# Optimization experiments

Hardware: AMD Instinct MI355X
Metric: run time of the kernel (lower is better)

The kernel has to match this reference:

```python
import jax, jax.numpy as jnp
import numpy as np

D_MODEL = 1024
N_HEADS = 16
D_KEYS = 64
D_LLM = 4096
B, L, S = 8, 1024, 1000
HD = N_HEADS * D_KEYS  # 1024


def setup_inputs() -> dict:
    key = jax.random.key(0)
    ks = jax.random.split(key, 12)
    sd = lambda fan_in: 1.0 / np.sqrt(fan_in)
    return {
        "target_embedding": jax.random.normal(ks[0], (B, L, D_MODEL), jnp.float32),
        "source_embedding": jax.random.normal(ks[1], (S, D_LLM), jnp.float32),
        "value_embedding": jax.random.normal(ks[2], (S, D_LLM), jnp.float32),
        "Wq": jax.random.normal(ks[3], (D_MODEL, HD), jnp.float32) * sd(D_MODEL),
        "bq": jnp.zeros((HD,), jnp.float32),
        "Wk": jax.random.normal(ks[4], (D_LLM, HD), jnp.float32) * sd(D_LLM),
        "bk": jnp.zeros((HD,), jnp.float32),
        "Wv": jax.random.normal(ks[5], (D_LLM, HD), jnp.float32) * sd(D_LLM),
        "bv": jnp.zeros((HD,), jnp.float32),
        "Wo": jax.random.normal(ks[6], (HD, D_LLM), jnp.float32) * sd(HD),
        "bo": jnp.zeros((D_LLM,), jnp.float32),
        "alpha": jnp.asarray(1.0, jnp.float32),
        "beta": jnp.asarray(0.5, jnp.float32),
    }


def reference(target_embedding, source_embedding, value_embedding,
              Wq, bq, Wk, bk, Wv, bv, Wo, bo, alpha, beta):
    # Projections
    q = (target_embedding @ Wq + bq).reshape(B, L, N_HEADS, D_KEYS)   # blhe
    k = (source_embedding @ Wk + bk).reshape(S, N_HEADS, D_KEYS)      # she
    v = (value_embedding @ Wv + bv).reshape(S, N_HEADS, D_KEYS)       # she
    # Reprogramming attention with alpha/beta scaling
    scale = 1.0 / np.sqrt(D_KEYS)
    scores = jnp.einsum('blhe,she->bhls', alpha * q, beta * k)        # BxHxLxS
    A = jax.nn.softmax(scale * scores, axis=-1)  # dropout is identity in eval
    out = jnp.einsum('bhls,she->blhe', A, v)
    out = out.reshape(B, L, HD)
    return out @ Wo + bo                                              # B,L,d_llm
```

## Files before the change

### kernel.cpp

```cpp
#include <hip/hip_runtime.h>

typedef unsigned short u16;
typedef __attribute__((ext_vector_type(8))) short short8;
typedef __attribute__((ext_vector_type(4))) float floatx4;

#define LOG2E 1.4426950408889634f

__device__ __forceinline__ u16 f2bf(float f) {
    unsigned u = __builtin_bit_cast(unsigned, f);
    u += 0x7fffu + ((u >> 16) & 1u);
    return (u16)(u >> 16);
}

__device__ __forceinline__ void gl2lds16(const void* g, void* l) {
    __builtin_amdgcn_global_load_lds((const __attribute__((address_space(1))) void*)g,
                                     (__attribute__((address_space(3))) void*)l,
                                     16, 0, 0);
}

__global__ __launch_bounds__(256) void conv_all(const float* __restrict__ T, u16* __restrict__ Tb,
                                                const float* __restrict__ Se, u16* __restrict__ Seb,
                                                const float* __restrict__ Ve, u16* __restrict__ Veb) {
    int g = blockIdx.x * 256 + threadIdx.x;
    const float* s; u16* d; int i; int nsrc;
    if (g < 2097152)      { s = T;  d = Tb;  i = g * 4;               nsrc = 8388608; }
    else if (g < 3145728) { s = Se; d = Seb; i = (g - 2097152) * 4;   nsrc = 4096000; }
    else                  { s = Ve; d = Veb; i = (g - 3145728) * 4;   nsrc = 4096000; }
    ushort4 o;
    if (i < nsrc) {
        float4 v = *(const float4*)(s + i);
        o.x = f2bf(v.x); o.y = f2bf(v.y); o.z = f2bf(v.z); o.w = f2bf(v.w);
    } else {
        o = make_ushort4(0, 0, 0, 0);
    }
    *(ushort4*)(d + i) = o;
}

__device__ __forceinline__ void transpose_core(const float* __restrict__ W, u16* __restrict__ Wt,
                                               int Kd, int Nd, int kx, int ny) {
    __shared__ u16 t[64][65];
    const int tid = threadIdx.x;
    const int k0 = kx * 64, n0 = ny * 64;
#pragma unroll
    for (int i = 0; i < 16; i++) {
        int r = i * 4 + (tid >> 6), c = tid & 63;
        t[r][c] = f2bf(W[(size_t)(k0 + r) * Nd + n0 + c]);
    }
    __syncthreads();
#pragma unroll
    for (int i = 0; i < 16; i++) {
        int n = i * 4 + (tid >> 6), k = tid & 63;
        Wt[(size_t)(n0 + n) * Kd + k0 + k] = t[k][n];
    }
}

__global__ __launch_bounds__(256) void transpose3(const float* __restrict__ Wq, u16* __restrict__ WqT,
                                                  const float* __restrict__ Wk, u16* __restrict__ WkT,
                                                  const float* __restrict__ Wv, u16* __restrict__ WvT) {
    int id = blockIdx.x;
    if (id < 256)       transpose_core(Wq, WqT, 1024, 1024, id & 15, id >> 4);
    else if (id < 1280) { int t = id - 256;  transpose_core(Wk, WkT, 4096, 1024, t & 63, t >> 6); }
    else                { int t = id - 1280; transpose_core(Wv, WvT, 4096, 1024, t & 63, t >> 6); }
}

__device__ __forceinline__
void gemm_core(const u16* __restrict__ A, const u16* __restrict__ Bt,
               const float* __restrict__ bias, void* __restrict__ Cout,
               int M, int N, int Kstride, int Klen, int koff,
               int mode, float mult, int m0, int n0,
               u16* sA, u16* sB) {
    const int tid = threadIdx.x;
    const int wave = tid >> 6, lane = tid & 63;
    const int quad = lane >> 4, l16 = lane & 15;
    const int wm = (wave >> 1) * 64, wn = (wave & 1) * 64;

    floatx4 acc[4][4];
#pragma unroll
    for (int i = 0; i < 4; i++)
#pragma unroll
        for (int j = 0; j < 4; j++) acc[i][j] = (floatx4){0.f, 0.f, 0.f, 0.f};

    const u16* Ag = A + (size_t)m0 * Kstride + koff;
    const u16* Bg = Bt + (size_t)n0 * Kstride + koff;
    const int sr = tid >> 3, sc = (tid & 7) * 8;

    for (int k0 = 0; k0 < Klen; k0 += 64) {
#pragma unroll
        for (int i = 0; i < 4; i++) {
            int r = i * 32 + sr;
            gl2lds16(Ag + (size_t)r * Kstride + k0 + sc, sA + i * 2048 + wave * 512);
            gl2lds16(Bg + (size_t)r * Kstride + k0 + sc, sB + i * 2048 + wave * 512);
        }
        __syncthreads();
#pragma unroll
        for (int kk = 0; kk < 64; kk += 32) {
            short8 af[4], bf[4];
#pragma unroll
            for (int i = 0; i < 4; i++)
                af[i] = *(const short8*)&sA[(wm + i * 16 + l16) * 64 + kk + quad * 8];
#pragma unroll
            for (int j = 0; j < 4; j++)
                bf[j] = *(const short8*)&sB[(wn + j * 16 + l16) * 64 + kk + quad * 8];
#pragma unroll
            for (int i = 0; i < 4; i++)
#pragma unroll
                for (int j = 0; j < 4; j++)
                    acc[i][j] = __builtin_amdgcn_mfma_f32_16x16x32_bf16(af[i], bf[j], acc[i][j], 0, 0, 0);
        }
        __syncthreads();
    }

#pragma unroll
    for (int i = 0; i < 4; i++) {
#pragma unroll
        for (int j = 0; j < 4; j++) {
            int col = n0 + wn + j * 16 + l16;
            float bv = (mode >= 4) ? 0.0f : bias[col];
#pragma unroll
            for (int r = 0; r < 4; r++) {
                int row = m0 + wm + i * 16 + quad * 4 + r;
                float v = (acc[i][j][r] + bv) * mult;
                if (mode == 3 || mode == 4) {
                    ((float*)Cout)[(size_t)row * N + col] = v;
                } else if (mode == 5) {
                    ((float*)Cout)[(size_t)col * M + row] = v;
                } else if (mode == 2) {
                    ((u16*)Cout)[(size_t)col * M + row] = f2bf(v);
                } else {
                    ((u16*)Cout)[(size_t)row * N + col] = f2bf(v);
                }
            }
        }
    }
}

__global__ __launch_bounds__(256, 2)
void gemm_qkv(const u16* __restrict__ Tb, const u16* __restrict__ WqT, const float* __restrict__ bq,
              const u16* __restrict__ Seb, const u16* __restrict__ WkT,
              const u16* __restrict__ Veb, const u16* __restrict__ WvT,
              u16* __restrict__ Qb, float* __restrict__ KP, float* __restrict__ VPT,
              const float* __restrict__ alphaP, const float* __restrict__ betaP) {
    __shared__ u16 sA[128 * 64];
    __shared__ u16 sB[128 * 64];
    int b0 = blockIdx.x;
    int bid = (b0 & 7) * 128 + (b0 >> 3);
    if (bid < 512) {
        int m = bid >> 3, n = bid & 7;
        float mult = alphaP[0] * betaP[0] * 0.125f * LOG2E;
        gemm_core(Tb, WqT, bq, Qb, 8192, 1024, 1024, 1024, 0,
                  1, mult, m * 128, n * 128, sA, sB);
    } else if (bid < 768) {
        int t = bid - 512;
        int kc = t >> 6, m = (t >> 3) & 7, n = t & 7;
        gemm_core(Seb, WkT, nullptr, KP + (size_t)kc * 1048576, 1024, 1024, 4096, 1024, kc * 1024,
                  4, 1.0f, m * 128, n * 128, sA, sB);
    } else {
        int t = bid - 768;
        int kc = t >> 6, m = (t >> 3) & 7, n = t & 7;
        gemm_core(Veb, WvT, nullptr, VPT + (size_t)kc * 1048576, 1024, 1024, 4096, 1024, kc * 1024,
                  5, 1.0f, m * 128, n * 128, sA, sB);
    }
}

__global__ __launch_bounds__(256)
void reduce_wo(const float* __restrict__ KP, const float* __restrict__ bk, u16* __restrict__ Kb,
               const float* __restrict__ VPT, const float* __restrict__ bv, u16* __restrict__ VTb,
               const float* __restrict__ Wo, u16* __restrict__ WoT) {
    int id = blockIdx.x;
    if (id >= 2048) {
        int t = id - 2048;
        transpose_core(Wo, WoT, 1024, 4096, t & 15, t >> 4);
        return;
    }
    const int tid = threadIdx.x;
    if (id < 1024) {
        int r = id, c = tid * 4;
        size_t base = (size_t)r * 1024 + c;
        float4 a0 = *(const float4*)(KP + base);
        float4 a1 = *(const float4*)(KP + 1048576 + base);
        float4 a2 = *(const float4*)(KP + 2097152 + base);
        float4 a3 = *(const float4*)(KP + 3145728 + base);
        float4 bb = *(const float4*)(bk + c);
        ushort4 o;
        o.x = f2bf(a0.x + a1.x + a2.x + a3.x + bb.x);
        o.y = f2bf(a0.y + a1.y + a2.y + a3.y + bb.y);
        o.z = f2bf(a0.z + a1.z + a2.z + a3.z + bb.z);
        o.w = f2bf(a0.w + a1.w + a2.w + a3.w + bb.w);
        *(ushort4*)(Kb + base) = o;
    } else {
        int d = id - 1024, s = tid * 4;
        size_t base = (size_t)d * 1024 + s;
        float4 a0 = *(const float4*)(VPT + base);
        float4 a1 = *(const float4*)(VPT + 1048576 + base);
        float4 a2 = *(const float4*)(VPT + 2097152 + base);
        float4 a3 = *(const float4*)(VPT + 3145728 + base);
        float bvv = bv[d];
        ushort4 o;
        o.x = f2bf(a0.x + a1.x + a2.x + a3.x + bvv);
        o.y = f2bf(a0.y + a1.y + a2.y + a3.y + bvv);
        o.z = f2bf(a0.z + a1.z + a2.z + a3.z + bvv);
        o.w = f2bf(a0.w + a1.w + a2.w + a3.w + bvv);
        *(ushort4*)(VTb + base) = o;
    }
}

__global__ __launch_bounds__(256, 2)
void gemm_final(const u16* __restrict__ A, const u16* __restrict__ Bt,
                const float* __restrict__ bias, float* __restrict__ Cout) {
    __shared__ u16 sA[128 * 64];
    __shared__ u16 sB[128 * 64];
    int b0 = blockIdx.x;
    int bid = (b0 & 7) * 256 + (b0 >> 3);
    int m = bid >> 5, n = bid & 31;
    gemm_core(A, Bt, bias, Cout, 8192, 4096, 1024, 1024, 0, 3, 1.0f, m * 128, n * 128, sA, sB);
}

__global__ __launch_bounds__(256, 2)
void attn_kernel(const u16* __restrict__ Q, const u16* __restrict__ Kb,
                 const u16* __restrict__ VT, u16* __restrict__ O) {
    __shared__ u16 sK[128 * 64];
    __shared__ u16 sV[64 * 128];
    __shared__ u16 sP[128 * 128];
    const int tid = threadIdx.x;
    const int wave = tid >> 6, lane = tid & 63;
    const int quad = lane >> 4, l16 = lane & 15;
    const int l7 = l16 & 7;
    const int bid = blockIdx.x;
    const int qt = bid & 7, h = (bid >> 3) & 15, b = bid >> 7;

    const u16* Qbase = Q + ((size_t)(b * 1024 + qt * 128 + wave * 32)) * 1024 + h * 64;
    short8 qf[2][2];
#pragma unroll
    for (int i = 0; i < 2; i++)
#pragma unroll
        for (int kk = 0; kk < 2; kk++)
            qf[i][kk] = *(const short8*)&Qbase[(size_t)(i * 16 + l16) * 1024 + kk * 32 + quad * 8];

    float psum[2] = {0.f, 0.f};
    floatx4 oacc[2][4];
#pragma unroll
    for (int i = 0; i < 2; i++)
#pragma unroll
        for (int n = 0; n < 4; n++) oacc[i][n] = (floatx4){0.f, 0.f, 0.f, 0.f};

    for (int st = 0; st < 8; ++st) {
#pragma unroll
        for (int i = 0; i < 4; i++) {
            int r = i * 32 + wave * 8 + (lane >> 3);
            int c = ((lane & 7) ^ ((lane >> 3) & 7)) * 8;
            gl2lds16(Kb + (size_t)(st * 128 + r) * 1024 + h * 64 + c, sK + i * 2048 + wave * 512);
        }
#pragma unroll
        for (int i = 0; i < 4; i++) {
            int r = i * 16 + wave * 4 + (lane >> 4);
            int c = ((lane & 15) ^ ((wave * 4 + (lane >> 4)) & 7)) * 8;
            gl2lds16(VT + (size_t)(h * 64 + r) * 1024 + st * 128 + c, sV + i * 2048 + wave * 512);
        }
        __syncthreads();

        floatx4 sacc[2][8];
#pragma unroll
        for (int i = 0; i < 2; i++)
#pragma unroll
            for (int j = 0; j < 8; j++) sacc[i][j] = (floatx4){0.f, 0.f, 0.f, 0.f};
#pragma unroll
        for (int kk = 0; kk < 2; kk++) {
            short8 kf[8];
#pragma unroll
            for (int j = 0; j < 8; j++)
                kf[j] = *(const short8*)&sK[(j * 16 + l16) * 64 + (((kk * 4 + quad) ^ l7) * 8)];
#pragma unroll
            for (int i = 0; i < 2; i++)
#pragma unroll
                for (int j = 0; j < 8; j++)
                    sacc[i][j] = __builtin_amdgcn_mfma_f32_16x16x32_bf16(kf[j], qf[i][kk], sacc[i][j], 0, 0, 0);
        }

#pragma unroll
        for (int i = 0; i < 2; i++) {
            const int rowbase = (wave * 32 + i * 16 + l16) * 128;
#pragma unroll
            for (int j = 0; j < 8; j++) {
                float p0 = exp2f(sacc[i][j][0]);
                float p1 = exp2f(sacc[i][j][1]);
                float p2 = exp2f(sacc[i][j][2]);
                float p3 = exp2f(sacc[i][j][3]);
                if (st == 7) {
                    if (j == 7 || (j == 6 && quad >= 2)) { p0 = p1 = p2 = p3 = 0.f; }
                }
                psum[i] += (p0 + p1) + (p2 + p3);
                uint2 val;
                val.x = (unsigned)f2bf(p0) | ((unsigned)f2bf(p1) << 16);
                val.y = (unsigned)f2bf(p2) | ((unsigned)f2bf(p3) << 16);
                int chunk = (2 * j + (quad >> 1)) ^ l7;
                *(uint2*)&sP[rowbase + chunk * 8 + (quad & 1) * 4] = val;
            }
        }

#pragma unroll
        for (int c = 0; c < 4; c++) {
            short8 pf[2], vf[4];
#pragma unroll
            for (int i = 0; i < 2; i++)
                pf[i] = *(const short8*)&sP[(wave * 32 + i * 16 + l16) * 128 + (((c * 4 + quad) ^ l7) * 8)];
#pragma unroll
            for (int n = 0; n < 4; n++)
                vf[n] = *(const short8*)&sV[(n * 16 + l16) * 128 + (((c * 4 + quad) ^ l7) * 8)];
#pragma unroll
            for (int i = 0; i < 2; i++)
#pragma unroll
                for (int n = 0; n < 4; n++)
                    oacc[i][n] = __builtin_amdgcn_mfma_f32_16x16x32_bf16(pf[i], vf[n], oacc[i][n], 0, 0, 0);
        }
        __syncthreads();
    }

#pragma unroll
    for (int i = 0; i < 2; i++) {
        psum[i] += __shfl_xor(psum[i], 16);
        psum[i] += __shfl_xor(psum[i], 32);
    }

    u16* Obase = O + ((size_t)(b * 1024 + qt * 128 + wave * 32)) * 1024 + h * 64;
#pragma unroll
    for (int i = 0; i < 2; i++) {
#pragma unroll
        for (int r = 0; r < 4; r++) {
            float l = __shfl(psum[i], (lane & 48) | (quad * 4 + r));
            float linv = 1.0f / l;
#pragma unroll
            for (int n = 0; n < 4; n++)
                Obase[(size_t)(i * 16 + quad * 4 + r) * 1024 + n * 16 + l16] = f2bf(oacc[i][n][r] * linv);
        }
    }
}

extern "C" void kernel_launch(void* const* d_in, const int* in_sizes, int n_in,
                              void* d_out, int out_size, void* d_ws, size_t ws_size,
                              hipStream_t stream) {
    const float* T     = (const float*)d_in[0];
    const float* Se    = (const float*)d_in[1];
    const float* Ve    = (const float*)d_in[2];
    const float* Wq    = (const float*)d_in[3];
    const float* bq    = (const float*)d_in[4];
    const float* Wk    = (const float*)d_in[5];
    const float* bk    = (const float*)d_in[6];
    const float* Wv    = (const float*)d_in[7];
    const float* bv    = (const float*)d_in[8];
    const float* Wo    = (const float*)d_in[9];
    const float* bo    = (const float*)d_in[10];
    const float* alpha = (const float*)d_in[11];
    const float* beta  = (const float*)d_in[12];

    char* ws = (char*)d_ws;
    size_t off = 0;
    auto alloc = [&](size_t bytes) { size_t o = off; off += (bytes + 255) & ~(size_t)255; return o; };

    u16* Tb  = (u16*)(ws + alloc((size_t)8192 * 1024 * 2));
    u16* Seb = (u16*)(ws + alloc((size_t)1024 * 4096 * 2));
    u16* Veb = (u16*)(ws + alloc((size_t)1024 * 4096 * 2));
    u16* WqT = (u16*)(ws + alloc((size_t)1024 * 1024 * 2));
    u16* WkT = (u16*)(ws + alloc((size_t)1024 * 4096 * 2));
    u16* WvT = (u16*)(ws + alloc((size_t)1024 * 4096 * 2));
    u16* Qb  = (u16*)(ws + alloc((size_t)8192 * 1024 * 2));
    u16* Kb  = (u16*)(ws + alloc((size_t)1024 * 1024 * 2));
    u16* VTb = (u16*)(ws + alloc((size_t)1024 * 1024 * 2));
    float* KP  = (float*)(ws + alloc((size_t)4 * 1024 * 1024 * 4));
    float* VPT = (float*)(ws + alloc((size_t)4 * 1024 * 1024 * 4));
    u16* Ob  = Tb;
    u16* WoT = Veb;

    conv_all<<<16384, 256, 0, stream>>>(T, Tb, Se, Seb, Ve, Veb);
    transpose3<<<2304, 256, 0, stream>>>(Wq, WqT, Wk, WkT, Wv, WvT);
    gemm_qkv<<<1024, 256, 0, stream>>>(Tb, WqT, bq, Seb, WkT, Veb, WvT,
                                       Qb, KP, VPT, alpha, beta);
    reduce_wo<<<3072, 256, 0, stream>>>(KP, bk, Kb, VPT, bv, VTb, Wo, WoT);
    attn_kernel<<<1024, 256, 0, stream>>>(Qb, Kb, VTb, Ob);
    gemm_final<<<2048, 256, 0, stream>>>(Ob, WoT, bo, (float*)d_out);
}
```

Before: 442.4 us.

## Rewrite GEMMs as 256x256 double-buffered 8-wave pipelined kernels with swizzled LDS

Replaces the 128x128 single-buffered GEMM core with a 256x256 tile computed by 8 waves, each holding an 8x4 MFMA accumulator block. Global-to-LDS loads for the next K-slab are issued inside a four-phase compute schedule using ping-pong buffers, with s_setprio around MFMA bursts. LDS rows are XOR-swizzled to avoid bank conflicts. The aim is to overlap memory with MFMA and raise data reuse per tile, at the cost of 128KB of LDS per block, fewer blocks (256 and 512), and more register pressure.

```diff
diff --git a/kernel.cpp b/kernel.cpp
--- a/kernel.cpp
+++ b/kernel.cpp
@@ -63,69 +63,154 @@
     else                { int t = id - 1280; transpose_core(Wv, WvT, 4096, 1024, t & 63, t >> 6); }
 }
 
+
+__device__ __forceinline__ short8 ldsfrag(const u16* b, int row, int kk, int quad, int l7) {
+    return *(const short8*)&b[row * 64 + (((kk * 4 + quad) ^ l7) * 8)];
+}
+
 __device__ __forceinline__
-void gemm_core(const u16* __restrict__ A, const u16* __restrict__ Bt,
-               const float* __restrict__ bias, void* __restrict__ Cout,
-               int M, int N, int Kstride, int Klen, int koff,
-               int mode, float mult, int m0, int n0,
-               u16* sA, u16* sB) {
+void stage_tile(u16* dA, u16* dB, const u16* gA, const u16* gB, int Ks, int wave, int lane) {
+    int rl = wave * 8 + (lane >> 3);
+    int cs = ((lane & 7) ^ (rl & 7)) * 8;
+#pragma unroll
+    for (int ii = 0; ii < 4; ii++) {
+        gl2lds16(gA + (size_t)(ii * 64 + rl) * Ks + cs, dA + ii * 4096 + wave * 512);
+        gl2lds16(gB + (size_t)(ii * 64 + rl) * Ks + cs, dB + ii * 4096 + wave * 512);
+    }
+}
+
+__device__ __forceinline__
+void four_phases(const u16* sA, const u16* sB, floatx4 (&acc)[8][4],
+                 int wm, int wn, int quad, int l16, int l7,
+                 bool stage, u16* dA, u16* dB, const u16* gA, const u16* gB, int Ks,
+                 int wave, int lane) {
+    short8 af[4][2], b0[2][2], b1[2][2];
+    const int ra = wm * 128 + l16, rb = wn * 64 + l16;
+
+#pragma unroll
+    for (int i = 0; i < 4; i++) {
+        af[i][0] = ldsfrag(sA, ra + i * 16, 0, quad, l7);
+        af[i][1] = ldsfrag(sA, ra + i * 16, 1, quad, l7);
+    }
+#pragma unroll
+    for (int j = 0; j < 2; j++) {
+        b0[j][0] = ldsfrag(sB, rb + j * 16, 0, quad, l7);
+        b0[j][1] = ldsfrag(sB, rb + j * 16, 1, quad, l7);
+    }
+    if (stage) stage_tile(dA, dB, gA, gB, Ks, wave, lane);
+    __builtin_amdgcn_s_barrier();
+    __builtin_amdgcn_s_setprio(1);
+#pragma unroll
+    for (int k = 0; k < 2; k++)
+#pragma unroll
+        for (int i = 0; i < 4; i++)
+#pragma unroll
+            for (int j = 0; j < 2; j++)
+                acc[i][j] = __builtin_amdgcn_mfma_f32_16x16x32_bf16(af[i][k], b0[j][k], acc[i][j], 0, 0, 0);
+    __builtin_amdgcn_s_setprio(0);
+    __builtin_amdgcn_s_barrier();
+
+#pragma unroll
+    for (int j = 0; j < 2; j++) {
+        b1[j][0] = ldsfrag(sB, rb + (j + 2) * 16, 0, quad, l7);
+        b1[j][1] = ldsfrag(sB, rb + (j + 2) * 16, 1, quad, l7);
+    }
+    __builtin_amdgcn_s_barrier();
+    __builtin_amdgcn_s_setprio(1);
+#pragma unroll
+    for (int k = 0; k < 2; k++)
+#pragma unroll
+        for (int i = 0; i < 4; i++)
+#pragma unroll
+            for (int j = 0; j < 2; j++)
+                acc[i][j + 2] = __builtin_amdgcn_mfma_f32_16x16x32_bf16(af[i][k], b1[j][k], acc[i][j + 2], 0, 0, 0);
+    __builtin_amdgcn_s_setprio(0);
+    __builtin_amdgcn_s_barrier();
+
+#pragma unroll
+    for (int i = 0; i < 4; i++) {
+        af[i][0] = ldsfrag(sA, ra + (i + 4) * 16, 0, quad, l7);
+        af[i][1] = ldsfrag(sA, ra + (i + 4) * 16, 1, quad, l7);
+    }
+    __builtin_amdgcn_s_barrier();
+    __builtin_amdgcn_s_setprio(1);
+#pragma unroll
+    for (int k = 0; k < 2; k++)
+#pragma unroll
+        for (int i = 0; i < 4; i++)
+#pragma unroll
+            for (int j = 0; j < 2; j++)
+                acc[i + 4][j + 2] = __builtin_amdgcn_mfma_f32_16x16x32_bf16(af[i][k], b1[j][k], acc[i + 4][j + 2], 0, 0, 0);
+    __builtin_amdgcn_s_setprio(0);
+    __builtin_amdgcn_s_barrier();
+
+    __builtin_amdgcn_s_setprio(1);
+#pragma unroll
+    for (int k = 0; k < 2; k++)
+#pragma unroll
+        for (int i = 0; i < 4; i++)
+#pragma unroll
+            for (int j = 0; j < 2; j++)
+                acc[i + 4][j] = __builtin_amdgcn_mfma_f32_16x16x32_bf16(af[i][k], b0[j][k], acc[i + 4][j], 0, 0, 0);
+    __builtin_amdgcn_s_setprio(0);
+}
+
+__device__ __forceinline__
+void gemm8_core(const u16* __restrict__ A, const u16* __restrict__ Bt,
+                const float* __restrict__ bias, void* __restrict__ Cout,
+                int M, int N, int Ks, int Klen, int koff,
+                int mode, float mult, int m0, int n0, u16* lds) {
     const int tid = threadIdx.x;
     const int wave = tid >> 6, lane = tid & 63;
-    const int quad = lane >> 4, l16 = lane & 15;
-    const int wm = (wave >> 1) * 64, wn = (wave & 1) * 64;
-
-    floatx4 acc[4][4];
-#pragma unroll
-    for (int i = 0; i < 4; i++)
+    const int quad = lane >> 4, l16 = lane & 15, l7 = l16 & 7;
+    const int wm = wave >> 2, wn = wave & 3;
+
+    u16* A0 = lds;          u16* B0 = lds + 16384;
+    u16* A1 = lds + 32768;  u16* B1 = lds + 49152;
+
+    floatx4 acc[8][4];
+#pragma unroll
+    for (int i = 0; i < 8; i++)
 #pragma unroll
         for (int j = 0; j < 4; j++) acc[i][j] = (floatx4){0.f, 0.f, 0.f, 0.f};
 
-    const u16* Ag = A + (size_t)m0 * Kstride + koff;
-    const u16* Bg = Bt + (size_t)n0 * Kstride + koff;
-    const int sr = tid >> 3, sc = (tid & 7) * 8;
-
-    for (int k0 = 0; k0 < Klen; k0 += 64) {
-#pragma unroll
-        for (int i = 0; i < 4; i++) {
-            int r = i * 32 + sr;
-            gl2lds16(Ag + (size_t)r * Kstride + k0 + sc, sA + i * 2048 + wave * 512);
-            gl2lds16(Bg + (size_t)r * Kstride + k0 + sc, sB + i * 2048 + wave * 512);
-        }
-        __syncthreads();
-#pragma unroll
-        for (int kk = 0; kk < 64; kk += 32) {
-            short8 af[4], bf[4];
-#pragma unroll
-            for (int i = 0; i < 4; i++)
-                af[i] = *(const short8*)&sA[(wm + i * 16 + l16) * 64 + kk + quad * 8];
-#pragma unroll
-            for (int j = 0; j < 4; j++)
-                bf[j] = *(const short8*)&sB[(wn + j * 16 + l16) * 64 + kk + quad * 8];
-#pragma unroll
-            for (int i = 0; i < 4; i++)
-#pragma unroll
-                for (int j = 0; j < 4; j++)
-                    acc[i][j] = __builtin_amdgcn_mfma_f32_16x16x32_bf16(af[i], bf[j], acc[i][j], 0, 0, 0);
-        }
-        __syncthreads();
-    }
-
-#pragma unroll
-    for (int i = 0; i < 4; i++) {
+    const u16* Ag = A + (size_t)m0 * Ks + koff;
+    const u16* Bg = Bt + (size_t)n0 * Ks + koff;
+
+    stage_tile(A0, B0, Ag, Bg, Ks, wave, lane);
+    asm volatile("s_waitcnt vmcnt(0)" ::: "memory");
+    __builtin_amdgcn_sched_barrier(0);
+    __builtin_amdgcn_s_barrier();
+
+    const int NIT = Klen >> 7;
+#pragma unroll 1
+    for (int it = 0; it < NIT; ++it) {
+        four_phases(A0, B0, acc, wm, wn, quad, l16, l7,
+                    true, A1, B1, Ag + (2 * it + 1) * 64, Bg + (2 * it + 1) * 64, Ks, wave, lane);
+        asm volatile("s_waitcnt vmcnt(0)" ::: "memory");
+        __builtin_amdgcn_sched_barrier(0);
+        __builtin_amdgcn_s_barrier();
+        four_phases(A1, B1, acc, wm, wn, quad, l16, l7,
+                    it + 1 < NIT, A0, B0, Ag + (2 * it + 2) * 64, Bg + (2 * it + 2) * 64, Ks, wave, lane);
+        asm volatile("s_waitcnt vmcnt(0)" ::: "memory");
+        __builtin_amdgcn_sched_barrier(0);
+        __builtin_amdgcn_s_barrier();
+    }
+
+#pragma unroll
+    for (int i = 0; i < 8; i++) {
 #pragma unroll
         for (int j = 0; j < 4; j++) {
-            int col = n0 + wn + j * 16 + l16;
-            float bv = (mode >= 4) ? 0.0f : bias[col];
+            int col = n0 + wn * 64 + j * 16 + l16;
+            float bvv = (mode >= 4) ? 0.0f : bias[col];
 #pragma unroll
             for (int r = 0; r < 4; r++) {
-                int row = m0 + wm + i * 16 + quad * 4 + r;
-                float v = (acc[i][j][r] + bv) * mult;
+                int row = m0 + wm * 128 + i * 16 + quad * 4 + r;
+                float v = (acc[i][j][r] + bvv) * mult;
                 if (mode == 3 || mode == 4) {
                     ((float*)Cout)[(size_t)row * N + col] = v;
                 } else if (mode == 5) {
                     ((float*)Cout)[(size_t)col * M + row] = v;
-                } else if (mode == 2) {
-                    ((u16*)Cout)[(size_t)col * M + row] = f2bf(v);
                 } else {
                     ((u16*)Cout)[(size_t)row * N + col] = f2bf(v);
                 }
@@ -134,32 +219,39 @@
     }
 }
 
-__global__ __launch_bounds__(256, 2)
+__global__ __launch_bounds__(512, 2)
 void gemm_qkv(const u16* __restrict__ Tb, const u16* __restrict__ WqT, const float* __restrict__ bq,
               const u16* __restrict__ Seb, const u16* __restrict__ WkT,
               const u16* __restrict__ Veb, const u16* __restrict__ WvT,
               u16* __restrict__ Qb, float* __restrict__ KP, float* __restrict__ VPT,
               const float* __restrict__ alphaP, const float* __restrict__ betaP) {
-    __shared__ u16 sA[128 * 64];
-    __shared__ u16 sB[128 * 64];
+    __shared__ u16 lds[65536];
     int b0 = blockIdx.x;
-    int bid = (b0 & 7) * 128 + (b0 >> 3);
-    if (bid < 512) {
-        int m = bid >> 3, n = bid & 7;
+    int w = (b0 & 7) * 32 + (b0 >> 3);
+    if (w < 128) {
         float mult = alphaP[0] * betaP[0] * 0.125f * LOG2E;
-        gemm_core(Tb, WqT, bq, Qb, 8192, 1024, 1024, 1024, 0,
-                  1, mult, m * 128, n * 128, sA, sB);
-    } else if (bid < 768) {
-        int t = bid - 512;
-        int kc = t >> 6, m = (t >> 3) & 7, n = t & 7;
-        gemm_core(Seb, WkT, nullptr, KP + (size_t)kc * 1048576, 1024, 1024, 4096, 1024, kc * 1024,
-                  4, 1.0f, m * 128, n * 128, sA, sB);
+        gemm8_core(Tb, WqT, bq, Qb, 8192, 1024, 1024, 1024, 0,
+                   1, mult, (w >> 2) * 256, (w & 3) * 256, lds);
+    } else if (w < 192) {
+        int t = w - 128; int kc = t >> 4;
+        gemm8_core(Seb, WkT, nullptr, KP + (size_t)kc * 1048576, 1024, 1024, 4096, 1024, kc * 1024,
+                   4, 1.0f, ((t >> 2) & 3) * 256, (t & 3) * 256, lds);
     } else {
-        int t = bid - 768;
-        int kc = t >> 6, m = (t >> 3) & 7, n = t & 7;
-        gemm_core(Veb, WvT, nullptr, VPT + (size_t)kc * 1048576, 1024, 1024, 4096, 1024, kc * 1024,
-                  5, 1.0f, m * 128, n * 128, sA, sB);
-    }
+        int t = w - 192; int kc = t >> 4;
+        gemm8_core(Veb, WvT, nullptr, VPT + (size_t)kc * 1048576, 1024, 1024, 4096, 1024, kc * 1024,
+                   5, 1.0f, ((t >> 2) & 3) * 256, (t & 3) * 256, lds);
+    }
+}
+
+__global__ __launch_bounds__(512, 2)
+void gemm_final(const u16* __restrict__ A, const u16* __restrict__ Bt,
+                const float* __restrict__ bias, float* __restrict__ Cout) {
+    __shared__ u16 lds[65536];
+    int b0 = blockIdx.x;
+    int idx = b0 >> 3;
+    int m = (b0 & 7) * 4 + (idx >> 4);
+    int n = idx & 15;
+    gemm8_core(A, Bt, bias, Cout, 8192, 4096, 1024, 1024, 0, 3, 1.0f, m * 256, n * 256, lds);
 }
 
 __global__ __launch_bounds__(256)
@@ -205,17 +297,6 @@
 }
 
 __global__ __launch_bounds__(256, 2)
-void gemm_final(const u16* __restrict__ A, const u16* __restrict__ Bt,
-                const float* __restrict__ bias, float* __restrict__ Cout) {
-    __shared__ u16 sA[128 * 64];
-    __shared__ u16 sB[128 * 64];
-    int b0 = blockIdx.x;
-    int bid = (b0 & 7) * 256 + (b0 >> 3);
-    int m = bid >> 5, n = bid & 31;
-    gemm_core(A, Bt, bias, Cout, 8192, 4096, 1024, 1024, 0, 3, 1.0f, m * 128, n * 128, sA, sB);
-}
-
-__global__ __launch_bounds__(256, 2)
 void attn_kernel(const u16* __restrict__ Q, const u16* __restrict__ Kb,
                  const u16* __restrict__ VT, u16* __restrict__ O) {
     __shared__ u16 sK[128 * 64];
@@ -372,9 +453,9 @@
 
     conv_all<<<16384, 256, 0, stream>>>(T, Tb, Se, Seb, Ve, Veb);
     transpose3<<<2304, 256, 0, stream>>>(Wq, WqT, Wk, WkT, Wv, WvT);
-    gemm_qkv<<<1024, 256, 0, stream>>>(Tb, WqT, bq, Seb, WkT, Veb, WvT,
-                                       Qb, KP, VPT, alpha, beta);
+    gemm_qkv<<<256, 512, 0, stream>>>(Tb, WqT, bq, Seb, WkT, Veb, WvT,
+                                      Qb, KP, VPT, alpha, beta);
     reduce_wo<<<3072, 256, 0, stream>>>(KP, bk, Kb, VPT, bv, VTb, Wo, WoT);
     attn_kernel<<<1024, 256, 0, stream>>>(Qb, Kb, VTb, Ob);
-    gemm_final<<<2048, 256, 0, stream>>>(Ob, WoT, bo, (float*)d_out);
-}
+    gemm_final<<<512, 512, 0, stream>>>(Ob, WoT, bo, (float*)d_out);
+}
```

After: 458.6 us. +3.7%, slower.
